# Optimization experiments

Measured on AMD Instinct MI355X. Metric: run time of the kernel, lower is better.

The kernel has to match this reference:

```python
import jax, jax.numpy as jnp
import numpy as np

TOP_K = 2


def setup_inputs() -> dict:
    key = jax.random.key(0)
    k1, k2, k3, k4 = jax.random.split(key, 4)
    B, N, D, E, F = 4, 2048, 1024, 8, 4096
    x = jax.random.normal(k1, (B, N, D), dtype=jnp.float32)
    gate_w = jax.random.normal(k2, (D, E), dtype=jnp.float32) * (D ** -0.5)
    w1 = jax.random.normal(k3, (E, D, F), dtype=jnp.float32) * (D ** -0.5)
    w2 = jax.random.normal(k4, (E, F, D), dtype=jnp.float32) * (F ** -0.5)
    return {"x": x, "gate_w": gate_w, "w1": w1, "w2": w2}


def reference(x, gate_w, w1, w2):
    # x: (B, N, D); gate_w: (D, E); w1: (E, D, F); w2: (E, F, D)
    E = gate_w.shape[-1]
    gate_logits = jnp.einsum("bnd,de->bne", x, gate_w)
    gate_probs = jax.nn.softmax(gate_logits, axis=-1)          # (B, N, E)
    top_k_probs, top_k_idx = jax.lax.top_k(gate_probs, TOP_K)   # (B, N, K)
    top_k_weights = top_k_probs / jnp.sum(top_k_probs, axis=-1, keepdims=True)
    # combined per-expert weight: sum_k w_k * onehot(idx_k) -> (B, N, E)
    comb = jnp.sum(jax.nn.one_hot(top_k_idx, E, dtype=x.dtype)
                   * top_k_weights[..., None], axis=2)
    # dense all-expert FFN (matches the torch masked-dense math exactly)
    h = jax.nn.gelu(jnp.einsum("bnd,edf->benf", x, w1))         # (B, E, N, F)
    expert_out = jnp.einsum("benf,efd->bend", h, w2)            # (B, E, N, D)
    output = jnp.einsum("bne,bend->bnd", comb, expert_out)      # (B, N, D)
    return output
```

## Files before the change

### kernel.cpp

```cpp
#include <hip/hip_runtime.h>
#include <hip/hip_bf16.h>

typedef short s16x8 __attribute__((ext_vector_type(8)));
typedef float f32x4 __attribute__((ext_vector_type(4)));
typedef float f32x2 __attribute__((ext_vector_type(2)));
typedef unsigned short us8 __attribute__((ext_vector_type(8)));
typedef unsigned short us4 __attribute__((ext_vector_type(4)));

#define T_TOK 8192
#define DDIM 1024
#define NEXP 8
#define FDIM 4096
#define MAXT 72
#define PADMAX (16384 + NEXP * 256)
#define GATHB ((PADMAX * 128) / 256)
#define TR1B 8192
#define TR2B 4096

#define GLOAD16(dst, src) \
  __builtin_amdgcn_global_load_lds((const __attribute__((address_space(1))) unsigned int*)(src), \
                                   (__attribute__((address_space(3))) unsigned int*)(dst), 16, 0, 0)
#define WAITVM(n) asm volatile("s_waitcnt vmcnt(" #n ")" ::: "memory")
#define MEMFENCE asm volatile("" ::: "memory")

__device__ __forceinline__ float gelu_fast(float x) {
  float x2 = x * x;
  float t = x * fmaf(x2, -0.07135532f, -1.5957691f);
  float e = __expf(t);
  return x * __builtin_amdgcn_rcpf(1.0f + e);
}
__device__ __forceinline__ float bf2f(unsigned short v) {
  return __uint_as_float((unsigned)v << 16);
}

__device__ __forceinline__ void trans64(const float* __restrict__ ip,
                                        __hip_bfloat16* __restrict__ op,
                                        int R, int C, int c0, int r0, int tid,
                                        __hip_bfloat16 (*tile)[66]) {
  int tx = tid & 31, ty = tid >> 5;
#pragma unroll
  for (int i = 0; i < 8; ++i) {
    int r = r0 + ty + i * 8;
    f32x2 v = __builtin_nontemporal_load(
        (const f32x2*)(ip + (size_t)r * C + c0 + tx * 2));
    tile[ty + i * 8][tx * 2]     = __float2bfloat16(v[0]);
    tile[ty + i * 8][tx * 2 + 1] = __float2bfloat16(v[1]);
  }
  __syncthreads();
#pragma unroll
  for (int i = 0; i < 8; ++i) {
    int cc = c0 + ty + i * 8;
    __hip_bfloat16 a = tile[tx * 2][ty + i * 8];
    __hip_bfloat16 b = tile[tx * 2 + 1][ty + i * 8];
    unsigned short ua = *(unsigned short*)&a, ub = *(unsigned short*)&b;
    unsigned int packed = (unsigned)ua | ((unsigned)ub << 16);
    *(unsigned int*)(op + (size_t)cc * R + r0 + tx * 2) = packed;
  }
}

__global__ __launch_bounds__(256) void gate_kernel(
    const float* __restrict__ x, const float* __restrict__ gw,
    int* __restrict__ tok_e, float* __restrict__ tok_w)
{
  int lane = threadIdx.x & 63;
  int tok = blockIdx.x * 4 + (threadIdx.x >> 6);
  const float* xr = x + (size_t)tok * DDIM;
  float acc[NEXP];
#pragma unroll
  for (int e = 0; e < NEXP; ++e) acc[e] = 0.f;
  for (int i = 0; i < DDIM / 64; ++i) {
    int d = i * 64 + lane;
    float xv = xr[d];
    const float* g = gw + (size_t)d * NEXP;
#pragma unroll
    for (int e = 0; e < NEXP; ++e) acc[e] += xv * g[e];
  }
#pragma unroll
  for (int off = 32; off > 0; off >>= 1) {
#pragma unroll
    for (int e = 0; e < NEXP; ++e) acc[e] += __shfl_xor(acc[e], off);
  }
  if (lane == 0) {
    int i1 = 0; float m1 = acc[0];
#pragma unroll
    for (int e = 1; e < NEXP; ++e) if (acc[e] > m1) { m1 = acc[e]; i1 = e; }
    int i2 = -1; float m2 = -3.4e38f;
#pragma unroll
    for (int e = 0; e < NEXP; ++e) if (e != i1 && acc[e] > m2) { m2 = acc[e]; i2 = e; }
    float w1 = 1.f / (1.f + expf(m2 - m1));
    tok_e[tok * 2] = i1; tok_e[tok * 2 + 1] = i2;
    tok_w[tok * 2] = w1; tok_w[tok * 2 + 1] = 1.f - w1;
  }
}

__global__ __launch_bounds__(256) void count_kernel(
    const int* __restrict__ tok_e, int* __restrict__ counts)
{
  __shared__ int lc[NEXP];
  if (threadIdx.x < NEXP) lc[threadIdx.x] = 0;
  __syncthreads();
  int tok = blockIdx.x * 256 + threadIdx.x;
  atomicAdd(&lc[tok_e[tok * 2]], 1);
  atomicAdd(&lc[tok_e[tok * 2 + 1]], 1);
  __syncthreads();
  if (threadIdx.x < NEXP) atomicAdd(&counts[threadIdx.x], lc[threadIdx.x]);
}

__global__ void scan_kernel(const int* __restrict__ counts, int* padded_off,
                            int* tile_e, int* tile_row, int* numTiles,
                            int* __restrict__ pair_token)
{
  if (blockIdx.x == 0) {
    for (int i = threadIdx.x; i < PADMAX; i += 256) pair_token[i] = -1;
    if (threadIdx.x == 0) {
      int off = 0, a = 0;
      for (int e = 0; e < NEXP; ++e) {
        padded_off[e] = off;
        int c = counts[e];
        int nt = (c + 255) / 256;
        for (int i = 0; i < nt; ++i) { tile_e[a] = e; tile_row[a] = off + i * 256; ++a; }
        off += nt * 256;
      }
      *numTiles = a;
    }
  }
}

__global__ __launch_bounds__(256) void scatter_kernel(
    const int* __restrict__ tok_e, const int* __restrict__ padded_off,
    int* __restrict__ fill, int* __restrict__ pair_token, int* __restrict__ tok_slot)
{
  __shared__ int lc[NEXP], lbase[NEXP];
  if (threadIdx.x < NEXP) lc[threadIdx.x] = 0;
  __syncthreads();
  int tok = blockIdx.x * 256 + threadIdx.x;
  int e0 = tok_e[tok * 2], e1 = tok_e[tok * 2 + 1];
  int r0 = atomicAdd(&lc[e0], 1);
  int r1 = atomicAdd(&lc[e1], 1);
  __syncthreads();
  if (threadIdx.x < NEXP) lbase[threadIdx.x] = atomicAdd(&fill[threadIdx.x], lc[threadIdx.x]);
  __syncthreads();
  int s0 = padded_off[e0] + lbase[e0] + r0;
  int s1 = padded_off[e1] + lbase[e1] + r1;
  pair_token[s0] = tok;
  pair_token[s1] = tok;
  tok_slot[tok * 2] = s0;
  tok_slot[tok * 2 + 1] = s1;
}

__global__ __launch_bounds__(256) void gather_trans1(
    const float* __restrict__ x, const int* __restrict__ pair_token,
    __hip_bfloat16* __restrict__ Xg,
    const float* __restrict__ w1, __hip_bfloat16* __restrict__ W1t)
{
  __shared__ __hip_bfloat16 tile[64][66];
  int bid = blockIdx.x;
  if (bid >= GATHB) {
    int i = bid - GATHB;
    int xq = i & 63, yq = (i >> 6) & 15, z = i >> 10;
    size_t mat = (size_t)DDIM * FDIM;
    trans64(w1 + (size_t)z * mat, W1t + (size_t)z * mat,
            DDIM, FDIM, xq * 64, yq * 64, threadIdx.x, tile);
    return;
  }
  int gid = bid * 256 + threadIdx.x;
  int r = gid >> 7;
  int c = (gid & 127) << 3;
  if (r >= PADMAX) return;
  int tk = pair_token[r];
  __hip_bfloat16 v[8];
  if (tk < 0) {
#pragma unroll
    for (int j = 0; j < 8; ++j) v[j] = __float2bfloat16(0.f);
  } else {
    const float* src = x + (size_t)tk * DDIM + c;
    f32x4 a = __builtin_nontemporal_load((const f32x4*)src);
    f32x4 b = __builtin_nontemporal_load((const f32x4*)(src + 4));
#pragma unroll
    for (int j = 0; j < 4; ++j) v[j] = __float2bfloat16(a[j]);
#pragma unroll
    for (int j = 0; j < 4; ++j) v[4 + j] = __float2bfloat16(b[j]);
  }
  *(us8*)(Xg + (size_t)r * DDIM + c) = *(const us8*)v;
}

template<int LD, int NT, int LDO, int NCOL, int SC, bool GELU, bool FUSET>
__global__ __launch_bounds__(512, 2) void moe_gemm8(
    const __hip_bfloat16* __restrict__ A, const __hip_bfloat16* __restrict__ B,
    __hip_bfloat16* __restrict__ Out,
    const int* __restrict__ tile_e, const int* __restrict__ tile_row,
    const int* __restrict__ numTiles,
    const float* __restrict__ w2, __hip_bfloat16* __restrict__ W2t)
{
  __shared__ __align__(16) __hip_bfloat16 lds[8][8192];
  if (FUSET && (int)blockIdx.x >= MAXT * NCOL) {
    int i2 = ((int)blockIdx.x - MAXT * NCOL) * 2 + (threadIdx.x >> 8);
    int xq = i2 & 15, yq = (i2 >> 4) & 63, z = i2 >> 10;
    int sub = threadIdx.x >> 8, tid = threadIdx.x & 255;
    __hip_bfloat16 (*tile)[66] =
        reinterpret_cast<__hip_bfloat16(*)[66]>(&lds[0][0] + sub * 64 * 66);
    size_t mat = (size_t)FDIM * DDIM;
    trans64(w2 + (size_t)z * mat, W2t + (size_t)z * mat,
            FDIM, DDIM, xq * 64, yq * 64, tid, tile);
    return;
  }
  constexpr int STU = 3 * SC;
  constexpr int NCG = NCOL / SC;
  const int bid = blockIdx.x;
  const int xcd = bid & 7;
  const int idx = bid >> 3;
  const int stg = idx / STU;
  const int within = idx % STU;
  const int colg = stg % NCG;
  const int tg = stg / NCG;
  const int tl = tg * 3 + within % 3;
  const int col = colg * SC + within / 3;
  const int nT = *numTiles;
  const int tile = ((xcd * nT) >> 3) + tl;
  if (tile >= (((xcd + 1) * nT) >> 3)) return;

  const int t = threadIdx.x, lane = t & 63, w = t >> 6;
  const int wm = w >> 2, wn = w & 3;
  const int fr = lane & 15, fkg = lane >> 4;
  const size_t rowoff = (size_t)(w * 8 + (lane >> 3)) * LD + (((lane & 7) ^ (lane >> 3)) << 3);
  const int aoff = (wm * 64 + fr) * 64;
  const int boff = (wn * 32 + fr) * 64;
  const int swk0 = (fkg ^ (fr & 7)) * 8;
  const int swk1 = ((4 + fkg) ^ (fr & 7)) * 8;

  const int e = tile_e[tile];
  const int row0 = tile_row[tile];
  const int col0 = col * 256;
  const __hip_bfloat16* Ab = A + (size_t)row0 * LD;
  const __hip_bfloat16* Bb = B + (size_t)e * ((size_t)FDIM * DDIM) + (size_t)col0 * LD;

  auto STAGEH = [&](const __hip_bfloat16* base, int mat, int half, int tt) {
    __hip_bfloat16* d = &lds[(((tt & 1) << 2) | (mat << 1) | half)][0] + w * 512;
    const __hip_bfloat16* s = base + (size_t)(half * 128) * LD + (size_t)tt * 64 + rowoff;
    GLOAD16(d, s);
    GLOAD16(d + 4096, s + (size_t)64 * LD);
  };

  f32x4 acc[4][4][2] = {};
  s16x8 af0[4][2], af1[4][2], b0[2][2], b1[2][2];

  STAGEH(Ab, 0, 0, 0); STAGEH(Bb, 1, 0, 0); STAGEH(Bb, 1, 1, 0); STAGEH(Ab, 0, 1, 0);
  STAGEH(Ab, 0, 0, 1);
  WAITVM(6);
  __builtin_amdgcn_s_barrier();
  MEMFENCE;
  {
    const __hip_bfloat16* A0r = &lds[0][0];
    const __hip_bfloat16* B0r = &lds[2][0];
#pragma unroll
    for (int m = 0; m < 4; ++m) {
      af0[m][0] = *(const s16x8*)(A0r + aoff + m * 1024 + swk0);
      af0[m][1] = *(const s16x8*)(A0r + aoff + m * 1024 + swk1);
    }
#pragma unroll
    for (int n = 0; n < 2; ++n) {
      b0[n][0] = *(const s16x8*)(B0r + boff + n * 1024 + swk0);
      b0[n][1] = *(const s16x8*)(B0r + boff + n * 1024 + swk1);
    }
  }

  for (int kt = 0; kt < NT; ++kt) {
    const int buf = kt & 1;
    const bool p1 = (kt + 1) < NT;
    const bool p2 = (kt + 2) < NT;
    const __hip_bfloat16* A1r = &lds[(buf << 2) | 1][0];
    const __hip_bfloat16* B1r = &lds[(buf << 2) | 3][0];
    const __hip_bfloat16* A0n = &lds[((buf ^ 1) << 2) | 0][0];
    const __hip_bfloat16* B0n = &lds[((buf ^ 1) << 2) | 2][0];

    if (p1) STAGEH(Bb, 1, 0, kt + 1);
    if (p1) { WAITVM(6); } else { WAITVM(2); }
    __builtin_amdgcn_s_barrier();
    MEMFENCE;
#pragma unroll
    for (int n = 0; n < 2; ++n) {
      b1[n][0] = *(const s16x8*)(B1r + boff + n * 1024 + swk0);
      b1[n][1] = *(const s16x8*)(B1r + boff + n * 1024 + swk1);
    }
    __builtin_amdgcn_s_setprio(1);
#pragma unroll
    for (int kk = 0; kk < 2; ++kk)
#pragma unroll
      for (int m = 0; m < 4; ++m)
#pragma unroll
        for (int n = 0; n < 2; ++n)
          acc[0][m][n] = __builtin_amdgcn_mfma_f32_16x16x32_bf16(af0[m][kk], b0[n][kk], acc[0][m][n], 0, 0, 0);
    __builtin_amdgcn_s_setprio(0);
    MEMFENCE;

    if (p1) STAGEH(Bb, 1, 1, kt + 1);
    if (p1) { WAITVM(6); } else { WAITVM(0); }
    __builtin_amdgcn_s_barrier();
    MEMFENCE;
#pragma unroll
    for (int m = 0; m < 4; ++m) {
      af1[m][0] = *(const s16x8*)(A1r + aoff + m * 1024 + swk0);
      af1[m][1] = *(const s16x8*)(A1r + aoff + m * 1024 + swk1);
    }
    __builtin_amdgcn_s_setprio(1);
#pragma unroll
    for (int kk = 0; kk < 2; ++kk)
#pragma unroll
      for (int m = 0; m < 4; ++m)
#pragma unroll
        for (int n = 0; n < 2; ++n)
          acc[1][m][n] = __builtin_amdgcn_mfma_f32_16x16x32_bf16(af0[m][kk], b1[n][kk], acc[1][m][n], 0, 0, 0);
    __builtin_amdgcn_s_setprio(0);
    MEMFENCE;

    if (p1) STAGEH(Ab, 0, 1, kt + 1);
    __builtin_amdgcn_s_barrier();
    MEMFENCE;
    __builtin_amdgcn_s_setprio(1);
#pragma unroll
    for (int kk = 0; kk < 2; ++kk)
#pragma unroll
      for (int m = 0; m < 4; ++m)
#pragma unroll
        for (int n = 0; n < 2; ++n)
          acc[3][m][n] = __builtin_amdgcn_mfma_f32_16x16x32_bf16(af1[m][kk], b0[n][kk], acc[3][m][n], 0, 0, 0);
    __builtin_amdgcn_s_setprio(0);
    MEMFENCE;

    if (p2) STAGEH(Ab, 0, 0, kt + 2);
    if (p1) { if (p2) { WAITVM(6); } else { WAITVM(4); } }
    __builtin_amdgcn_s_barrier();
    MEMFENCE;
    if (p1) {
#pragma unroll
      for (int m = 0; m < 4; ++m) {
        af0[m][0] = *(const s16x8*)(A0n + aoff + m * 1024 + swk0);
        af0[m][1] = *(const s16x8*)(A0n + aoff + m * 1024 + swk1);
      }
#pragma unroll
      for (int n = 0; n < 2; ++n) {
        b0[n][0] = *(const s16x8*)(B0n + boff + n * 1024 + swk0);
        b0[n][1] = *(const s16x8*)(B0n + boff + n * 1024 + swk1);
      }
    }
    __builtin_amdgcn_s_setprio(1);
#pragma unroll
    for (int kk = 0; kk < 2; ++kk)
#pragma unroll
      for (int m = 0; m < 4; ++m)
#pragma unroll
        for (int n = 0; n < 2; ++n)
          acc[2][m][n] = __builtin_amdgcn_mfma_f32_16x16x32_bf16(af1[m][kk], b1[n][kk], acc[2][m][n], 0, 0, 0);
    __builtin_amdgcn_s_setprio(0);
    MEMFENCE;
  }

  const int cbase = col0 + wn * 32 + fr;
#pragma unroll
  for (int mh = 0; mh < 2; ++mh) {
    const int qa = mh ? 3 : 0;
    const int qb = mh ? 2 : 1;
#pragma unroll
    for (int m = 0; m < 4; ++m) {
#pragma unroll
      for (int j = 0; j < 4; ++j) {
        int r = row0 + mh * 128 + wm * 64 + m * 16 + fkg * 4 + j;
        __hip_bfloat16* p = Out + (size_t)r * LDO + cbase;
        float v0 = acc[qa][m][0][j];
        float v1 = acc[qa][m][1][j];
        float v2 = acc[qb][m][0][j];
        float v3 = acc[qb][m][1][j];
        if (GELU) {
          v0 = gelu_fast(v0); v1 = gelu_fast(v1);
          v2 = gelu_fast(v2); v3 = gelu_fast(v3);
        }
        p[0]   = __float2bfloat16(v0);
        p[16]  = __float2bfloat16(v1);
        p[128] = __float2bfloat16(v2);
        p[144] = __float2bfloat16(v3);
      }
    }
  }
}

__global__ __launch_bounds__(256) void combine_kernel(
    const __hip_bfloat16* __restrict__ Eout, const int* __restrict__ tok_slot,
    const float* __restrict__ tok_w, float* __restrict__ out)
{
  int tok = blockIdx.x;
  int sa = tok_slot[tok * 2], sb = tok_slot[tok * 2 + 1];
  float wa = tok_w[tok * 2], wb = tok_w[tok * 2 + 1];
  const __hip_bfloat16* ra = Eout + (size_t)sa * DDIM;
  const __hip_bfloat16* rb = Eout + (size_t)sb * DDIM;
  float* op = out + (size_t)tok * DDIM;
  int c = threadIdx.x * 4;
  us4 va = *(const us4*)(ra + c);
  us4 vb = *(const us4*)(rb + c);
  float4 o;
  o.x = wa * bf2f(va.x) + wb * bf2f(vb.x);
  o.y = wa * bf2f(va.y) + wb * bf2f(vb.y);
  o.z = wa * bf2f(va.z) + wb * bf2f(vb.z);
  o.w = wa * bf2f(va.w) + wb * bf2f(vb.w);
  *(float4*)(op + c) = o;
}

extern "C" void kernel_launch(void* const* d_in, const int* in_sizes, int n_in,
                              void* d_out, int out_size, void* d_ws, size_t ws_size,
                              hipStream_t stream)
{
  const float* x      = (const float*)d_in[0];
  const float* gate_w = (const float*)d_in[1];
  const float* w1     = (const float*)d_in[2];
  const float* w2     = (const float*)d_in[3];
  float* out = (float*)d_out;

  char* ws = (char*)d_ws;
  size_t off = 0;
  auto alloc = [&](size_t bytes) -> void* {
    void* p = ws + off;
    off = (off + bytes + 255) & ~(size_t)255;
    return p;
  };
  int* ctrl = (int*)alloc(1024);
  int* counts     = ctrl + 0;
  int* fill       = ctrl + 8;
  int* padded_off = ctrl + 16;
  int* numTiles   = ctrl + 24;
  int*   tile_e     = (int*)alloc(MAXT * 4);
  int*   tile_row   = (int*)alloc(MAXT * 4);
  int*   tok_e      = (int*)alloc((size_t)T_TOK * 2 * 4);
  float* tok_w      = (float*)alloc((size_t)T_TOK * 2 * 4);
  int*   tok_slot   = (int*)alloc((size_t)T_TOK * 2 * 4);
  int*   pair_token = (int*)alloc((size_t)PADMAX * 4);
  __hip_bfloat16* XgEout = (__hip_bfloat16*)alloc((size_t)PADMAX * DDIM * 2);
  __hip_bfloat16* W1t  = (__hip_bfloat16*)alloc((size_t)NEXP * FDIM * DDIM * 2);
  __hip_bfloat16* W2t  = (__hip_bfloat16*)alloc((size_t)NEXP * FDIM * DDIM * 2);
  __hip_bfloat16* Hbuf = (__hip_bfloat16*)alloc((size_t)PADMAX * FDIM * 2);
  (void)in_sizes; (void)n_in; (void)ws_size; (void)out_size;

  (void)hipMemsetAsync(d_ws, 0, 1024, stream);

  gate_kernel<<<T_TOK / 4, 256, 0, stream>>>(x, gate_w, tok_e, tok_w);
  count_kernel<<<T_TOK / 256, 256, 0, stream>>>(tok_e, counts);
  scan_kernel<<<1, 256, 0, stream>>>(counts, padded_off, tile_e, tile_row, numTiles,
                                     pair_token);
  scatter_kernel<<<T_TOK / 256, 256, 0, stream>>>(tok_e, padded_off, fill,
                                                  pair_token, tok_slot);
  gather_trans1<<<GATHB + TR1B, 256, 0, stream>>>(x, pair_token, XgEout, w1, W1t);

  moe_gemm8<DDIM, DDIM / 64, FDIM, FDIM / 256, 8, true, true>
      <<<MAXT * (FDIM / 256) + TR2B, 512, 0, stream>>>(XgEout, W1t, Hbuf,
                                                       tile_e, tile_row, numTiles,
                                                       w2, W2t);
  moe_gemm8<FDIM, FDIM / 64, DDIM, DDIM / 256, 4, false, false>
      <<<MAXT * (DDIM / 256), 512, 0, stream>>>(Hbuf, W2t, XgEout,
                                                tile_e, tile_row, numTiles,
                                                nullptr, nullptr);

  combine_kernel<<<T_TOK, 256, 0, stream>>>(XgEout, tok_slot, tok_w, out);
}
```

Measured before the change: 472.3 us.

## Split-K the second expert GEMM into four partitions reduced in combine

The down-projection GEMM (K=4096, only 4 output column blocks per tile) is split along K into four parts, so four times as many workgroups run, each writing a bf16 partial output to its own buffer. The combine kernel now sums the four partials for each of a token's two expert slots before applying the routing weights. This targets low occupancy in the second GEMM, where few tiles times four columns underfill the GPU. The cost is four times the partial-output write and read traffic, plus extra bf16 rounding on each partial.

New measurement: 451.4 us. 1.05x faster.

```diff
diff --git a/kernel.cpp b/kernel.cpp
--- a/kernel.cpp
+++ b/kernel.cpp
@@ -184,17 +184,19 @@
   *(us8*)(Xg + (size_t)r * DDIM + c) = *(const us8*)v;
 }
 
-template<int LD, int NT, int LDO, int NCOL, int SC, bool GELU, bool FUSET>
+template<int LD, int NT, int LDO, int NCOL, int PARTS, int SC, bool GELU, bool FUSET>
 __global__ __launch_bounds__(512, 2) void moe_gemm8(
     const __hip_bfloat16* __restrict__ A, const __hip_bfloat16* __restrict__ B,
     __hip_bfloat16* __restrict__ Out,
     const int* __restrict__ tile_e, const int* __restrict__ tile_row,
     const int* __restrict__ numTiles,
-    const float* __restrict__ w2, __hip_bfloat16* __restrict__ W2t)
+    const float* __restrict__ w2, __hip_bfloat16* __restrict__ W2t,
+    size_t pstride)
 {
   __shared__ __align__(16) __hip_bfloat16 lds[8][8192];
-  if (FUSET && (int)blockIdx.x >= MAXT * NCOL) {
-    int i2 = ((int)blockIdx.x - MAXT * NCOL) * 2 + (threadIdx.x >> 8);
+  constexpr int NCP = NCOL * PARTS;
+  if (FUSET && (int)blockIdx.x >= MAXT * NCP) {
+    int i2 = ((int)blockIdx.x - MAXT * NCP) * 2 + (threadIdx.x >> 8);
     int xq = i2 & 15, yq = (i2 >> 4) & 63, z = i2 >> 10;
     int sub = threadIdx.x >> 8, tid = threadIdx.x & 255;
     __hip_bfloat16 (*tile)[66] =
@@ -205,7 +207,7 @@
     return;
   }
   constexpr int STU = 3 * SC;
-  constexpr int NCG = NCOL / SC;
+  constexpr int NCG = NCP / SC;
   const int bid = blockIdx.x;
   const int xcd = bid & 7;
   const int idx = bid >> 3;
@@ -214,7 +216,9 @@
   const int colg = stg % NCG;
   const int tg = stg / NCG;
   const int tl = tg * 3 + within % 3;
-  const int col = colg * SC + within / 3;
+  const int colp = colg * SC + within / 3;
+  const int col = colp % NCOL;
+  const int part = colp / NCOL;
   const int nT = *numTiles;
   const int tile = ((xcd * nT) >> 3) + tl;
   if (tile >= (((xcd + 1) * nT) >> 3)) return;
@@ -231,8 +235,9 @@
   const int e = tile_e[tile];
   const int row0 = tile_row[tile];
   const int col0 = col * 256;
-  const __hip_bfloat16* Ab = A + (size_t)row0 * LD;
-  const __hip_bfloat16* Bb = B + (size_t)e * ((size_t)FDIM * DDIM) + (size_t)col0 * LD;
+  const size_t koff = (size_t)part * (LD / PARTS);
+  const __hip_bfloat16* Ab = A + (size_t)row0 * LD + koff;
+  const __hip_bfloat16* Bb = B + (size_t)e * ((size_t)FDIM * DDIM) + (size_t)col0 * LD + koff;
 
   auto STAGEH = [&](const __hip_bfloat16* base, int mat, int half, int tt) {
     __hip_bfloat16* d = &lds[(((tt & 1) << 2) | (mat << 1) | half)][0] + w * 512;
@@ -355,6 +360,7 @@
     MEMFENCE;
   }
 
+  __hip_bfloat16* Ob = Out + (size_t)part * pstride;
   const int cbase = col0 + wn * 32 + fr;
 #pragma unroll
   for (int mh = 0; mh < 2; ++mh) {
@@ -365,7 +371,7 @@
 #pragma unroll
       for (int j = 0; j < 4; ++j) {
         int r = row0 + mh * 128 + wm * 64 + m * 16 + fkg * 4 + j;
-        __hip_bfloat16* p = Out + (size_t)r * LDO + cbase;
+        __hip_bfloat16* p = Ob + (size_t)r * LDO + cbase;
         float v0 = acc[qa][m][0][j];
         float v1 = acc[qa][m][1][j];
         float v2 = acc[qb][m][0][j];
@@ -384,23 +390,28 @@
 }
 
 __global__ __launch_bounds__(256) void combine_kernel(
-    const __hip_bfloat16* __restrict__ Eout, const int* __restrict__ tok_slot,
+    const __hip_bfloat16* __restrict__ E, const int* __restrict__ tok_slot,
     const float* __restrict__ tok_w, float* __restrict__ out)
 {
+  const size_t PS = (size_t)PADMAX * DDIM;
   int tok = blockIdx.x;
   int sa = tok_slot[tok * 2], sb = tok_slot[tok * 2 + 1];
   float wa = tok_w[tok * 2], wb = tok_w[tok * 2 + 1];
-  const __hip_bfloat16* ra = Eout + (size_t)sa * DDIM;
-  const __hip_bfloat16* rb = Eout + (size_t)sb * DDIM;
   float* op = out + (size_t)tok * DDIM;
   int c = threadIdx.x * 4;
-  us4 va = *(const us4*)(ra + c);
-  us4 vb = *(const us4*)(rb + c);
+  float oa[4] = {0.f, 0.f, 0.f, 0.f}, ob[4] = {0.f, 0.f, 0.f, 0.f};
+#pragma unroll
+  for (int p = 0; p < 4; ++p) {
+    us4 va = *(const us4*)(E + p * PS + (size_t)sa * DDIM + c);
+    us4 vb = *(const us4*)(E + p * PS + (size_t)sb * DDIM + c);
+#pragma unroll
+    for (int j = 0; j < 4; ++j) { oa[j] += bf2f(va[j]); ob[j] += bf2f(vb[j]); }
+  }
   float4 o;
-  o.x = wa * bf2f(va.x) + wb * bf2f(vb.x);
-  o.y = wa * bf2f(va.y) + wb * bf2f(vb.y);
-  o.z = wa * bf2f(va.z) + wb * bf2f(vb.z);
-  o.w = wa * bf2f(va.w) + wb * bf2f(vb.w);
+  o.x = wa * oa[0] + wb * ob[0];
+  o.y = wa * oa[1] + wb * ob[1];
+  o.z = wa * oa[2] + wb * ob[2];
+  o.w = wa * oa[3] + wb * ob[3];
   *(float4*)(op + c) = o;
 }
 
@@ -432,7 +443,8 @@
   float* tok_w      = (float*)alloc((size_t)T_TOK * 2 * 4);
   int*   tok_slot   = (int*)alloc((size_t)T_TOK * 2 * 4);
   int*   pair_token = (int*)alloc((size_t)PADMAX * 4);
-  __hip_bfloat16* XgEout = (__hip_bfloat16*)alloc((size_t)PADMAX * DDIM * 2);
+  __hip_bfloat16* EoutAll = (__hip_bfloat16*)alloc((size_t)4 * PADMAX * DDIM * 2);
+  __hip_bfloat16* Xg = EoutAll;
   __hip_bfloat16* W1t  = (__hip_bfloat16*)alloc((size_t)NEXP * FDIM * DDIM * 2);
   __hip_bfloat16* W2t  = (__hip_bfloat16*)alloc((size_t)NEXP * FDIM * DDIM * 2);
   __hip_bfloat16* Hbuf = (__hip_bfloat16*)alloc((size_t)PADMAX * FDIM * 2);
@@ -446,16 +458,17 @@
                                      pair_token);
   scatter_kernel<<<T_TOK / 256, 256, 0, stream>>>(tok_e, padded_off, fill,
                                                   pair_token, tok_slot);
-  gather_trans1<<<GATHB + TR1B, 256, 0, stream>>>(x, pair_token, XgEout, w1, W1t);
-
-  moe_gemm8<DDIM, DDIM / 64, FDIM, FDIM / 256, 8, true, true>
-      <<<MAXT * (FDIM / 256) + TR2B, 512, 0, stream>>>(XgEout, W1t, Hbuf,
+  gather_trans1<<<GATHB + TR1B, 256, 0, stream>>>(x, pair_token, Xg, w1, W1t);
+
+  moe_gemm8<DDIM, DDIM / 64, FDIM, FDIM / 256, 1, 8, true, true>
+      <<<MAXT * (FDIM / 256) + TR2B, 512, 0, stream>>>(Xg, W1t, Hbuf,
                                                        tile_e, tile_row, numTiles,
-                                                       w2, W2t);
-  moe_gemm8<FDIM, FDIM / 64, DDIM, DDIM / 256, 4, false, false>
-      <<<MAXT * (DDIM / 256), 512, 0, stream>>>(Hbuf, W2t, XgEout,
-                                                tile_e, tile_row, numTiles,
-                                                nullptr, nullptr);
-
-  combine_kernel<<<T_TOK, 256, 0, stream>>>(XgEout, tok_slot, tok_w, out);
-}
+                                                       w2, W2t, 0);
+  moe_gemm8<FDIM, FDIM / 64 / 4, DDIM, DDIM / 256, 4, 4, false, false>
+      <<<MAXT * (DDIM / 256) * 4, 512, 0, stream>>>(Hbuf, W2t, EoutAll,
+                                                    tile_e, tile_row, numTiles,
+                                                    nullptr, nullptr,
+                                                    (size_t)PADMAX * DDIM);
+
+  combine_kernel<<<T_TOK, 256, 0, stream>>>(EoutAll, tok_slot, tok_w, out);
+}
```
